# Kernel optimization log

Hardware: AMD Instinct MI355X
Metric: run time of the kernel (lower is better)

Reference implementation:

```python
import jax, jax.numpy as jnp
import numpy as np

INPUT_DIM, QK_DIM, V_DIM = 1024, 512, 512

def setup_inputs() -> dict:
    key = jax.random.key(0)
    ks = jax.random.split(key, 7)
    B, S = 4, 2048
    scale = 1.0 / np.sqrt(INPUT_DIM)
    return {
        "x": jax.random.normal(ks[0], (B, S, INPUT_DIM), dtype=jnp.float32),
        "Wq": jax.random.normal(ks[1], (INPUT_DIM, QK_DIM), dtype=jnp.float32) * scale,
        "bq": jax.random.normal(ks[2], (QK_DIM,), dtype=jnp.float32) * 0.01,
        "Wk": jax.random.normal(ks[3], (INPUT_DIM, QK_DIM), dtype=jnp.float32) * scale,
        "bk": jax.random.normal(ks[4], (QK_DIM,), dtype=jnp.float32) * 0.01,
        "Wv": jax.random.normal(ks[5], (INPUT_DIM, V_DIM), dtype=jnp.float32) * scale,
        "bv": jax.random.normal(ks[6], (V_DIM,), dtype=jnp.float32) * 0.01,
    }

def reference(x, Wq, bq, Wk, bk, Wv, bv):
    # q,k: (B,S,Dqk), v: (B,S,Dv)
    q = jnp.einsum("bsi,id->bsd", x, Wq) + bq
    k = jnp.einsum("bsi,id->bsd", x, Wk) + bk
    v = jnp.einsum("bsi,id->bsd", x, Wv) + bv
    scale = 1.0 / jnp.sqrt(jnp.asarray(q.shape[-1], q.dtype))
    scores = jnp.einsum("bqd,bkd->bqk", q, k) * scale  # (B,S,S)
    attn = jax.nn.softmax(scores, axis=-1)
    return jnp.einsum("bqk,bkd->bqd", attn, v)
```

## Files before the change

### kernel.cpp

```cpp
#include <hip/hip_runtime.h>

typedef __attribute__((ext_vector_type(8))) short short8;
typedef __attribute__((ext_vector_type(4))) float f32x4;

#define S_    2048
#define DI    1024
#define DQK   512
#define DV    512
#define NTOK  8192

#define GLL(gp, lp) __builtin_amdgcn_global_load_lds( \
    (const __attribute__((address_space(1))) unsigned int*)(gp), \
    (__attribute__((address_space(3))) unsigned int*)(lp), 16, 0, 0)

static __device__ __forceinline__ unsigned short f2bf(float f) {
  unsigned int u = __float_as_uint(f);
  u += 0x7fffu + ((u >> 16) & 1u);
  return (unsigned short)(u >> 16);
}

__global__ void conv_x_kernel(const float* __restrict__ x,
                              unsigned short* __restrict__ xb, int n) {
  int idx = (blockIdx.x * 256 + threadIdx.x) * 8;
  if (idx >= n) return;
  const float4* p = (const float4*)(x + idx);
  float4 f0 = p[0], f1 = p[1];
  uint4 o;
  o.x = (unsigned)f2bf(f0.x) | ((unsigned)f2bf(f0.y) << 16);
  o.y = (unsigned)f2bf(f0.z) | ((unsigned)f2bf(f0.w) << 16);
  o.z = (unsigned)f2bf(f1.x) | ((unsigned)f2bf(f1.y) << 16);
  o.w = (unsigned)f2bf(f1.z) | ((unsigned)f2bf(f1.w) << 16);
  *(uint4*)(xb + idx) = o;
}

__global__ void conv_wT_kernel(const float* __restrict__ W0, const float* __restrict__ W1,
                               const float* __restrict__ W2,
                               unsigned short* __restrict__ T0, unsigned short* __restrict__ T1,
                               unsigned short* __restrict__ T2,
                               float* __restrict__ rowsum) {
  __shared__ float tile[32][33];
  int mat = blockIdx.z;
  if (mat == 0 && blockIdx.x == 0)
    rowsum[blockIdx.y * 256 + threadIdx.x] = 0.f;
  const float* W = (mat == 0) ? W0 : (mat == 1) ? W1 : W2;
  unsigned short* T = (mat == 0) ? T0 : (mat == 1) ? T1 : T2;
  int n0 = blockIdx.x * 32, k0 = blockIdx.y * 32;
  int c = threadIdx.x & 31, r0 = threadIdx.x >> 5;
  for (int i = 0; i < 4; ++i) {
    int kk = r0 + i * 8;
    tile[kk][c] = W[(k0 + kk) * DQK + n0 + c];
  }
  __syncthreads();
  for (int i = 0; i < 4; ++i) {
    int nn = r0 + i * 8;
    T[(n0 + nn) * DI + k0 + c] = f2bf(tile[c][nn]);
  }
}

__device__ __forceinline__ void gemm_core_128x128(
    const unsigned short* __restrict__ A, const unsigned short* __restrict__ B,
    int lda, int ldb, int K, int m0, int n0,
    unsigned short* As, unsigned short* Bs, f32x4 (&acc)[4][4]) {
  int tid = threadIdx.x, lane = tid & 63, wv = tid >> 6;
  int quad = lane >> 4, l16 = lane & 15;
  int wm = wv >> 1, wn = wv & 1;
  int r0 = wv * 32 + (lane >> 2);
  int c8 = ((lane & 3) ^ ((lane >> 2) & 3)) * 8;
  const unsigned short* ga0 = A + (size_t)(m0 + r0) * lda + c8;
  const unsigned short* ga1 = ga0 + (size_t)16 * lda;
  const unsigned short* gb0 = B + (size_t)(n0 + r0) * ldb + c8;
  const unsigned short* gb1 = gb0 + (size_t)16 * ldb;
  int ldsw0 = (wv * 32) * 32;
  int ldsw1 = ldsw0 + 16 * 32;
#pragma unroll
  for (int i = 0; i < 4; ++i)
#pragma unroll
    for (int j = 0; j < 4; ++j) acc[i][j] = (f32x4){0.f, 0.f, 0.f, 0.f};

  auto stage = [&](int buf, int k0) {
    unsigned short* Ad = As + buf * (128 * 32);
    unsigned short* Bd = Bs + buf * (128 * 32);
    GLL(ga0 + k0, Ad + ldsw0);
    GLL(ga1 + k0, Ad + ldsw1);
    GLL(gb0 + k0, Bd + ldsw0);
    GLL(gb1 + k0, Bd + ldsw1);
  };

  int nk = K >> 5;
  int pc = (quad ^ (l16 & 3)) * 8;
  stage(0, 0);
  for (int kt = 0; kt < nk; ++kt) {
    int cur = kt & 1;
    __syncthreads();
    if (kt + 1 < nk) stage(cur ^ 1, (kt + 1) * 32);
    const unsigned short* Ab = As + cur * (128 * 32);
    const unsigned short* Bb = Bs + cur * (128 * 32);
    short8 af[4], bf[4];
#pragma unroll
    for (int t = 0; t < 4; ++t) {
      af[t] = *(const short8*)(Ab + (wm * 64 + t * 16 + l16) * 32 + pc);
      bf[t] = *(const short8*)(Bb + (wn * 64 + t * 16 + l16) * 32 + pc);
    }
#pragma unroll
    for (int tm = 0; tm < 4; ++tm)
#pragma unroll
      for (int tn = 0; tn < 4; ++tn)
        acc[tm][tn] = __builtin_amdgcn_mfma_f32_16x16x32_bf16(af[tm], bf[tn], acc[tm][tn], 0, 0, 0);
  }
}

__global__ __launch_bounds__(256, 2) void qkv_dma_kernel(
    const unsigned short* __restrict__ xb,
    const unsigned short* __restrict__ wqt, const unsigned short* __restrict__ wkt,
    const unsigned short* __restrict__ wvt,
    const float* __restrict__ bq, const float* __restrict__ bk, const float* __restrict__ bv,
    unsigned short* __restrict__ qo, unsigned short* __restrict__ ko,
    unsigned short* __restrict__ vto) {
  __shared__ unsigned short As[2 * 128 * 32];
  __shared__ unsigned short Bs[2 * 128 * 32];
  int bidx = blockIdx.x;
  int xcd = bidx & 7;
  int local = bidx >> 3;
  int mlocal = local & 7;
  int col12 = local >> 3;
  int mat = col12 >> 2;
  int m0 = (xcd * 8 + mlocal) * 128;
  int n0 = (col12 & 3) * 128;
  const unsigned short* wt = (mat == 0) ? wqt : (mat == 1) ? wkt : wvt;
  const float* bias = (mat == 0) ? bq : (mat == 1) ? bk : bv;
  float oscale = (mat == 0) ? 0.04419417382415922f : 1.0f;
  f32x4 acc[4][4];
  gemm_core_128x128(xb, wt, DI, DI, DI, m0, n0, As, Bs, acc);

  int tid = threadIdx.x, lane = tid & 63, wv = tid >> 6;
  int quad = lane >> 4, l16 = lane & 15;
  int wm = wv >> 1, wn = wv & 1;
  bool transp = (mat == 2);
  unsigned short* outp = (mat == 0) ? qo : (mat == 1) ? ko : vto;
#pragma unroll
  for (int tn = 0; tn < 4; ++tn) {
    int col = n0 + wn * 64 + tn * 16 + l16;
    float bc = bias[col];
#pragma unroll
    for (int tm = 0; tm < 4; ++tm) {
      int rowb = m0 + wm * 64 + tm * 16 + quad * 4;
      f32x4 a = acc[tm][tn];
      if (!transp) {
        outp[(size_t)(rowb + 0) * DQK + col] = f2bf((a.x + bc) * oscale);
        outp[(size_t)(rowb + 1) * DQK + col] = f2bf((a.y + bc) * oscale);
        outp[(size_t)(rowb + 2) * DQK + col] = f2bf((a.z + bc) * oscale);
        outp[(size_t)(rowb + 3) * DQK + col] = f2bf((a.w + bc) * oscale);
      } else {
        ushort4 pk;
        pk.x = f2bf(a.x + bc); pk.y = f2bf(a.y + bc);
        pk.z = f2bf(a.z + bc); pk.w = f2bf(a.w + bc);
        *(ushort4*)(outp + (size_t)col * NTOK + rowb) = pk;
      }
    }
  }
}

__global__ __launch_bounds__(256, 2) void s_exp_kernel(
    const unsigned short* __restrict__ q, const unsigned short* __restrict__ k,
    unsigned short* __restrict__ sp, float* __restrict__ rowsum) {
  __shared__ unsigned short As[2 * 128 * 32];
  __shared__ unsigned short Bs[2 * 128 * 32];
  int bidx = blockIdx.x;
  int xcd = bidx & 7, b = xcd >> 1;
  int sub = ((bidx >> 3) << 1) | (xcd & 1);
  int m0 = (sub >> 4) * 128, n0 = (sub & 15) * 128;
  f32x4 acc[4][4];
  gemm_core_128x128(k + (size_t)b * S_ * DQK, q + (size_t)b * S_ * DQK,
                    DQK, DQK, DQK, m0, n0, As, Bs, acc);

  int tid = threadIdx.x, lane = tid & 63, wv = tid >> 6;
  int quad = lane >> 4, l16 = lane & 15;
  int wm = wv >> 1, wn = wv & 1;
  unsigned short* Cb = sp + (size_t)b * S_ * S_;
#pragma unroll
  for (int tn = 0; tn < 4; ++tn) {
    int qrow = n0 + wn * 64 + tn * 16 + l16;
    float rs = 0.f;
#pragma unroll
    for (int tm = 0; tm < 4; ++tm) {
      int kcol = m0 + wm * 64 + tm * 16 + quad * 4;
      f32x4 a = acc[tm][tn];
      float e0 = __expf(a.x), e1 = __expf(a.y), e2 = __expf(a.z), e3 = __expf(a.w);
      ushort4 pk;
      pk.x = f2bf(e0); pk.y = f2bf(e1); pk.z = f2bf(e2); pk.w = f2bf(e3);
      *(ushort4*)(Cb + (size_t)qrow * S_ + kcol) = pk;
      rs += (e0 + e1) + (e2 + e3);
    }
    rs += __shfl_xor(rs, 16);
    rs += __shfl_xor(rs, 32);
    if (quad == 0) atomicAdd(rowsum + b * S_ + qrow, rs);
  }
}

__global__ __launch_bounds__(256, 4) void pv_kernel(
    const unsigned short* __restrict__ sp, const unsigned short* __restrict__ vt,
    const float* __restrict__ rowsum, float* __restrict__ out) {
  __shared__ unsigned short As[2][64 * 64];
  __shared__ unsigned short Bs[2][64 * 64];
  int bidx = blockIdx.x;
  int xcd = bidx & 7, b = xcd >> 1;
  int sub = ((bidx >> 3) << 1) | (xcd & 1);
  int m0 = (sub >> 3) * 64, n0 = (sub & 7) * 64;
  int tid = threadIdx.x, lane = tid & 63, wv = tid >> 6;
  int quad = lane >> 4, l16 = lane & 15;
  int wm = wv >> 1, wn = wv & 1;
  const unsigned short* A = sp + (size_t)b * S_ * S_;
  const unsigned short* B = vt + (size_t)b * S_;

  int srow = tid >> 3;
  int schunk = (tid & 7) ^ (srow & 7);
  const unsigned short* gA0 = A + (size_t)(m0 + srow) * S_ + schunk * 8;
  const unsigned short* gA1 = A + (size_t)(m0 + 32 + srow) * S_ + schunk * 8;
  const unsigned short* gB0 = B + (size_t)(n0 + srow) * NTOK + schunk * 8;
  const unsigned short* gB1 = B + (size_t)(n0 + 32 + srow) * NTOK + schunk * 8;
  int ldsw0 = (wv * 8) * 64;
  int ldsw1 = (32 + wv * 8) * 64;

  f32x4 acc[2][2];
#pragma unroll
  for (int i = 0; i < 2; ++i)
#pragma unroll
    for (int j = 0; j < 2; ++j) acc[i][j] = (f32x4){0.f, 0.f, 0.f, 0.f};

  auto stage = [&](int buf, int k0) {
    GLL(gA0 + k0, &As[buf][ldsw0]);
    GLL(gA1 + k0, &As[buf][ldsw1]);
    GLL(gB0 + k0, &Bs[buf][ldsw0]);
    GLL(gB1 + k0, &Bs[buf][ldsw1]);
  };

  stage(0, 0);
  for (int kt = 0; kt < 32; ++kt) {
    int cur = kt & 1;
    __syncthreads();
    if (kt + 1 < 32) stage(cur ^ 1, (kt + 1) * 64);
#pragma unroll
    for (int ks = 0; ks < 2; ++ks) {
      int pc = ((ks * 4 + quad) ^ (l16 & 7)) * 8;
      short8 af[2], bf[2];
#pragma unroll
      for (int t = 0; t < 2; ++t) {
        af[t] = *(const short8*)(&As[cur][(wm * 32 + t * 16 + l16) * 64 + pc]);
        bf[t] = *(const short8*)(&Bs[cur][(wn * 32 + t * 16 + l16) * 64 + pc]);
      }
#pragma unroll
      for (int tm = 0; tm < 2; ++tm)
#pragma unroll
        for (int tn = 0; tn < 2; ++tn)
          acc[tm][tn] = __builtin_amdgcn_mfma_f32_16x16x32_bf16(af[tm], bf[tn], acc[tm][tn], 0, 0, 0);
    }
  }

  float* ob = out + (size_t)b * S_ * DV;
#pragma unroll
  for (int tm = 0; tm < 2; ++tm) {
    int rowb = m0 + wm * 32 + tm * 16 + quad * 4;
    float inv[4];
#pragma unroll
    for (int i = 0; i < 4; ++i) inv[i] = 1.0f / rowsum[b * S_ + rowb + i];
#pragma unroll
    for (int tn = 0; tn < 2; ++tn) {
      int col = n0 + wn * 32 + tn * 16 + l16;
      f32x4 a = acc[tm][tn];
      ob[(size_t)(rowb + 0) * DV + col] = a.x * inv[0];
      ob[(size_t)(rowb + 1) * DV + col] = a.y * inv[1];
      ob[(size_t)(rowb + 2) * DV + col] = a.z * inv[2];
      ob[(size_t)(rowb + 3) * DV + col] = a.w * inv[3];
    }
  }
}

extern "C" void kernel_launch(void* const* d_in, const int* in_sizes, int n_in,
                              void* d_out, int out_size, void* d_ws, size_t ws_size,
                              hipStream_t stream) {
  const float* x  = (const float*)d_in[0];
  const float* Wq = (const float*)d_in[1];
  const float* bq = (const float*)d_in[2];
  const float* Wk = (const float*)d_in[3];
  const float* bk = (const float*)d_in[4];
  const float* Wv = (const float*)d_in[5];
  const float* bv = (const float*)d_in[6];
  float* out = (float*)d_out;

  char* ws = (char*)d_ws;
  unsigned short* xb  = (unsigned short*)(ws);
  unsigned short* wqt = (unsigned short*)(ws + 16777216);
  unsigned short* wkt = (unsigned short*)(ws + 16777216 + 1048576);
  unsigned short* wvt = (unsigned short*)(ws + 16777216 + 2097152);
  unsigned short* qo  = (unsigned short*)(ws + 19922944);
  unsigned short* ko  = (unsigned short*)(ws + 19922944 + 8388608);
  unsigned short* vto = (unsigned short*)(ws + 19922944 + 16777216);
  unsigned short* sp  = (unsigned short*)(ws + 45088768);
  float* rowsum       = (float*)(ws + 45088768 + 33554432);

  conv_x_kernel<<<4096, 256, 0, stream>>>(x, xb, NTOK * DI);
  dim3 gw(16, 32, 3);
  conv_wT_kernel<<<gw, 256, 0, stream>>>(Wq, Wk, Wv, wqt, wkt, wvt, rowsum);
  qkv_dma_kernel<<<768, 256, 0, stream>>>(xb, wqt, wkt, wvt, bq, bk, bv, qo, ko, vto);
  s_exp_kernel<<<1024, 256, 0, stream>>>(qo, ko, sp, rowsum);
  pv_kernel<<<1024, 256, 0, stream>>>(sp, vto, rowsum, out);
}
```

Before: 182.3 us.

## Triple-buffer GEMM LDS pipeline and merge conversion kernels into one launch

```diff
diff --git a/kernel.cpp b/kernel.cpp
--- a/kernel.cpp
+++ b/kernel.cpp
@@ -19,27 +19,29 @@
   return (unsigned short)(u >> 16);
 }
 
-__global__ void conv_x_kernel(const float* __restrict__ x,
-                              unsigned short* __restrict__ xb, int n) {
-  int idx = (blockIdx.x * 256 + threadIdx.x) * 8;
-  if (idx >= n) return;
-  const float4* p = (const float4*)(x + idx);
-  float4 f0 = p[0], f1 = p[1];
-  uint4 o;
-  o.x = (unsigned)f2bf(f0.x) | ((unsigned)f2bf(f0.y) << 16);
-  o.y = (unsigned)f2bf(f0.z) | ((unsigned)f2bf(f0.w) << 16);
-  o.z = (unsigned)f2bf(f1.x) | ((unsigned)f2bf(f1.y) << 16);
-  o.w = (unsigned)f2bf(f1.z) | ((unsigned)f2bf(f1.w) << 16);
-  *(uint4*)(xb + idx) = o;
-}
-
-__global__ void conv_wT_kernel(const float* __restrict__ W0, const float* __restrict__ W1,
-                               const float* __restrict__ W2,
-                               unsigned short* __restrict__ T0, unsigned short* __restrict__ T1,
-                               unsigned short* __restrict__ T2,
-                               float* __restrict__ rowsum) {
+__global__ void conv_all_kernel(const float* __restrict__ x,
+                                const float* __restrict__ W0, const float* __restrict__ W1,
+                                const float* __restrict__ W2,
+                                unsigned short* __restrict__ xb,
+                                unsigned short* __restrict__ T0, unsigned short* __restrict__ T1,
+                                unsigned short* __restrict__ T2,
+                                float* __restrict__ rowsum) {
+  int z = blockIdx.z;
+  if (z >= 3) {
+    int blk = (z - 3) * 512 + blockIdx.y * 16 + blockIdx.x;
+    int idx = (blk * 256 + threadIdx.x) * 8;
+    const float4* p = (const float4*)(x + idx);
+    float4 f0 = p[0], f1 = p[1];
+    uint4 o;
+    o.x = (unsigned)f2bf(f0.x) | ((unsigned)f2bf(f0.y) << 16);
+    o.y = (unsigned)f2bf(f0.z) | ((unsigned)f2bf(f0.w) << 16);
+    o.z = (unsigned)f2bf(f1.x) | ((unsigned)f2bf(f1.y) << 16);
+    o.w = (unsigned)f2bf(f1.z) | ((unsigned)f2bf(f1.w) << 16);
+    *(uint4*)(xb + idx) = o;
+    return;
+  }
   __shared__ float tile[32][33];
-  int mat = blockIdx.z;
+  int mat = z;
   if (mat == 0 && blockIdx.x == 0)
     rowsum[blockIdx.y * 256 + threadIdx.x] = 0.f;
   const float* W = (mat == 0) ? W0 : (mat == 1) ? W1 : W2;
@@ -89,10 +91,16 @@
   int nk = K >> 5;
   int pc = (quad ^ (l16 & 3)) * 8;
   stage(0, 0);
+  stage(1, 32);
+  int cur = 0, pre = 2;
   for (int kt = 0; kt < nk; ++kt) {
-    int cur = kt & 1;
-    __syncthreads();
-    if (kt + 1 < nk) stage(cur ^ 1, (kt + 1) * 32);
+    if (kt + 1 < nk) { asm volatile("s_waitcnt vmcnt(4)" ::: "memory"); }
+    else             { asm volatile("s_waitcnt vmcnt(0)" ::: "memory"); }
+    __builtin_amdgcn_sched_barrier(0);
+    __builtin_amdgcn_s_barrier();
+    __builtin_amdgcn_sched_barrier(0);
+    if (kt + 2 < nk) stage(pre, (kt + 2) * 32);
+    __builtin_amdgcn_sched_barrier(0);
     const unsigned short* Ab = As + cur * (128 * 32);
     const unsigned short* Bb = Bs + cur * (128 * 32);
     short8 af[4], bf[4];
@@ -106,6 +114,8 @@
 #pragma unroll
       for (int tn = 0; tn < 4; ++tn)
         acc[tm][tn] = __builtin_amdgcn_mfma_f32_16x16x32_bf16(af[tm], bf[tn], acc[tm][tn], 0, 0, 0);
+    cur = (cur == 2) ? 0 : cur + 1;
+    pre = (pre == 2) ? 0 : pre + 1;
   }
 }
 
@@ -116,8 +126,8 @@
     const float* __restrict__ bq, const float* __restrict__ bk, const float* __restrict__ bv,
     unsigned short* __restrict__ qo, unsigned short* __restrict__ ko,
     unsigned short* __restrict__ vto) {
-  __shared__ unsigned short As[2 * 128 * 32];
-  __shared__ unsigned short Bs[2 * 128 * 32];
+  __shared__ unsigned short As[3 * 128 * 32];
+  __shared__ unsigned short Bs[3 * 128 * 32];
   int bidx = blockIdx.x;
   int xcd = bidx & 7;
   int local = bidx >> 3;
@@ -163,8 +173,8 @@
 __global__ __launch_bounds__(256, 2) void s_exp_kernel(
     const unsigned short* __restrict__ q, const unsigned short* __restrict__ k,
     unsigned short* __restrict__ sp, float* __restrict__ rowsum) {
-  __shared__ unsigned short As[2 * 128 * 32];
-  __shared__ unsigned short Bs[2 * 128 * 32];
+  __shared__ unsigned short As[3 * 128 * 32];
+  __shared__ unsigned short Bs[3 * 128 * 32];
   int bidx = blockIdx.x;
   int xcd = bidx & 7, b = xcd >> 1;
   int sub = ((bidx >> 3) << 1) | (xcd & 1);
@@ -298,9 +308,8 @@
   unsigned short* sp  = (unsigned short*)(ws + 45088768);
   float* rowsum       = (float*)(ws + 45088768 + 33554432);
 
-  conv_x_kernel<<<4096, 256, 0, stream>>>(x, xb, NTOK * DI);
-  dim3 gw(16, 32, 3);
-  conv_wT_kernel<<<gw, 256, 0, stream>>>(Wq, Wk, Wv, wqt, wkt, wvt, rowsum);
+  dim3 gc(16, 32, 11);
+  conv_all_kernel<<<gc, 256, 0, stream>>>(x, Wq, Wk, Wv, xb, wqt, wkt, wvt, rowsum);
   qkv_dma_kernel<<<768, 256, 0, stream>>>(xb, wqt, wkt, wvt, bq, bk, bv, qo, ko, vto);
   s_exp_kernel<<<1024, 256, 0, stream>>>(qo, ko, sp, rowsum);
   pv_kernel<<<1024, 256, 0, stream>>>(sp, vto, rowsum, out);
```

New measurement: 180.5 us. Within noise of the previous version (-1.0%).
